# Kernel optimization log

Hardware: AMD Instinct MI355X
Metric: run time of the kernel (lower is better)

The kernel has to match this reference:

```python
import jax, jax.numpy as jnp
import numpy as np

NEG_INF = -9e15  # same masking constant as the torch module


def setup_inputs() -> dict:
    key = jax.random.key(0)
    k1, k2, k3 = jax.random.split(key, 3)
    B, S, F = 8, 2048, 128
    H, D = 4, 32  # n_heads, head_dim = out_features // n_heads
    features = jax.random.normal(k1, (B, S, F), dtype=jnp.float32)
    adj_matrix = jax.random.randint(k2, (B, S, S), 0, 2, dtype=jnp.int32)
    # Xavier-uniform-ish init for W [H, F, D]
    limit = float(np.sqrt(6.0 / (F + D)))
    W = jax.random.uniform(k3, (H, F, D), dtype=jnp.float32, minval=-limit, maxval=limit)
    return {"features": features, "adj_matrix": adj_matrix, "W": W}


def reference(features, adj_matrix, W):
    # features: [B, S, F], adj_matrix: [B, S, S] (>0 == edge), W: [H, F, D]
    D = W.shape[-1]
    Wh = jnp.einsum("bsf,hfd->bhsd", features, W)                 # [B, H, S, D]
    scores = jnp.einsum("bhsd,bhtd->bhst", Wh, Wh) / jnp.sqrt(jnp.float32(D))
    scores = jnp.where(adj_matrix[:, None, :, :] > 0, scores, NEG_INF)
    attn = jax.nn.softmax(scores, axis=-1)                         # [B, H, S, S]
    # dropout is identity at inference (training=False)
    h = jnp.einsum("bhst,bhtd->bhsd", attn, Wh)                    # [B, H, S, D]
    B, H, S, _ = h.shape
    # concat heads along feature dim, matching torch.cat(heads, dim=2)
    return jnp.transpose(h, (0, 2, 1, 3)).reshape(B, S, H * D)
```

## Files before the change

kernel.cpp:

```cpp
#include <hip/hip_runtime.h>
#include <hip/hip_bf16.h>
#include <stdint.h>


namespace {
constexpr int S = 2048;
constexpr int F = 128;
constexpr int H = 4;
constexpr int D = 32;

typedef __attribute__((ext_vector_type(4))) float f32x4;
typedef __attribute__((ext_vector_type(8))) short s16x8;
typedef __attribute__((ext_vector_type(4))) short s16x4;

__device__ __forceinline__ short f2bf(float f) {
  __hip_bfloat16 h = __float2bfloat16(f);
  short s; __builtin_memcpy(&s, &h, sizeof(s)); return s;
}
__device__ __forceinline__ float bf2f(short s) {
  __hip_bfloat16 h; __builtin_memcpy(&h, &s, sizeof(s));
  return __bfloat162float(h);
}

__global__ __launch_bounds__(256) void gat_proj(const float* __restrict__ feat,
                                                const float* __restrict__ W,
                                                short* __restrict__ Wh,
                                                short* __restrict__ WhT) {
  __shared__ __align__(16) short ftile[64][136];
  const int tid = threadIdx.x;
  const int w = tid >> 6;
  const int l = tid & 63;
  const int ln = l & 15, lg = l >> 4, g4 = (l >> 4) * 4;
  const int row0 = blockIdx.x * 64;
  const int b = row0 >> 11;
  const int sl0 = row0 & (S - 1);

#pragma unroll
  for (int i = 0; i < 4; ++i) {
    int c = i * 256 + tid;
    int r = c >> 4, c8 = (c & 15) * 8;
    const float* src = feat + (size_t)(row0 + r) * F + c8;
    float4 v0 = *(const float4*)src;
    float4 v1 = *(const float4*)(src + 4);
    s16x8 v;
    v[0]=f2bf(v0.x); v[1]=f2bf(v0.y); v[2]=f2bf(v0.z); v[3]=f2bf(v0.w);
    v[4]=f2bf(v1.x); v[5]=f2bf(v1.y); v[6]=f2bf(v1.z); v[7]=f2bf(v1.w);
    *(s16x8*)&ftile[r][c8] = v;
  }

  s16x8 bfr[4][2];
#pragma unroll
  for (int ks = 0; ks < 4; ++ks)
#pragma unroll
    for (int nt = 0; nt < 2; ++nt) {
      s16x8 v;
#pragma unroll
      for (int j = 0; j < 8; ++j)
        v[j] = f2bf(W[((size_t)w * F + ks*32 + lg*8 + j) * D + nt*16 + ln]);
      bfr[ks][nt] = v;
    }
  __syncthreads();

  const f32x4 z4 = {0.f, 0.f, 0.f, 0.f};
#pragma unroll
  for (int mt = 0; mt < 4; ++mt) {
    s16x8 a[4];
#pragma unroll
    for (int ks = 0; ks < 4; ++ks)
      a[ks] = *(const s16x8*)&ftile[mt*16 + ln][ks*32 + lg*8];
#pragma unroll
    for (int nt = 0; nt < 2; ++nt) {
      f32x4 c = z4;
#pragma unroll
      for (int ks = 0; ks < 4; ++ks)
        c = __builtin_amdgcn_mfma_f32_16x16x32_bf16(a[ks], bfr[ks][nt], c, 0, 0, 0);
      s16x4 tv;
#pragma unroll
      for (int r = 0; r < 4; ++r) {
        tv[r] = f2bf(c[r]);
        int srow = row0 + mt*16 + g4 + r;
        int s = srow & (S - 1);
        Wh[(((size_t)b * H + w) * S + s) * D + nt*16 + ln] = tv[r];
      }
      *(s16x4*)&WhT[(((size_t)b * H + w) * D + nt*16 + ln) * S + sl0 + mt*16 + g4] = tv;
    }
  }
}

__global__ __launch_bounds__(256, 2) void gat_attn(const int* __restrict__ adj,
                                                   const short* __restrict__ Wh,
                                                   const short* __restrict__ WhT,
                                                   float* __restrict__ out) {
  __shared__ unsigned adjw[2][32][20];
  __shared__ __align__(16) short ptl[H][32][64];

  const int tid = threadIdx.x;
  const int w = tid >> 6;
  const int l = tid & 63;
  const int ln = l & 15, lg = l >> 4, g4 = (l >> 4) * 4;
  const int e3 = ln & 7;
  const int b = blockIdx.x >> 6;
  const int s0 = (blockIdx.x & 63) * 32;

  const short* WhBH = Wh + ((size_t)b * H + w) * S * D;
  const short* WhTBH = WhT + ((size_t)b * H + w) * D * S;
  const int* adjB = adj + (size_t)b * S * S;
  short* pw = &ptl[w][0][0];

  const int ra = tid >> 4;
  const int cg = tid & 15;
  const int* adjR0 = adjB + (size_t)(s0 + ra) * S + cg * 4;
  const int* adjR1 = adjB + (size_t)(s0 + 16 + ra) * S + cg * 4;

  const float cs = 0.25503486f;
  s16x8 qf[2];
#pragma unroll
  for (int qt = 0; qt < 2; ++qt) {
    s16x8 v = *(const s16x8*)&WhBH[(size_t)(s0 + qt*16 + ln) * D + lg*8];
    s16x8 o;
#pragma unroll
    for (int j = 0; j < 8; ++j) o[j] = f2bf(bf2f(v[j]) * cs);
    qf[qt] = o;
  }

  const f32x4 z4 = {0.f, 0.f, 0.f, 0.f};
  f32x4 accO[2][2];
#pragma unroll
  for (int i = 0; i < 2; ++i)
#pragma unroll
    for (int j = 0; j < 2; ++j) accO[i][j] = z4;
  float psum[2] = {0.f, 0.f};

  int4 a0 = *(const int4*)adjR0;
  int4 a1 = *(const int4*)adjR1;
  s16x8 kf[4];
#pragma unroll
  for (int mt = 0; mt < 4; ++mt)
    kf[mt] = *(const s16x8*)&WhBH[(size_t)(mt*16 + ln) * D + lg*8];
  s16x8 av[2][2];
#pragma unroll
  for (int dt = 0; dt < 2; ++dt)
#pragma unroll
    for (int kt = 0; kt < 2; ++kt)
      av[dt][kt] = *(const s16x8*)&WhTBH[(size_t)(dt*16 + ln) * S + kt*32 + lg*8];
  adjw[0][ra][cg]      = (unsigned)a0.x | ((unsigned)a0.y << 8) |
                         ((unsigned)a0.z << 16) | ((unsigned)a0.w << 24);
  adjw[0][16 + ra][cg] = (unsigned)a1.x | ((unsigned)a1.y << 8) |
                         ((unsigned)a1.z << 16) | ((unsigned)a1.w << 24);
  __syncthreads();

#pragma unroll 1
  for (int it = 0; it < S / 64; ++it) {
    const int cur = it & 1, nxt = cur ^ 1;
    const int t0n = (it + 1) * 64;
    const bool pf = (it < S / 64 - 1);

    int4 a0n, a1n;
    s16x8 kn[4], avn[2][2];
    if (pf) {
      a0n = *(const int4*)(adjR0 + t0n);
      a1n = *(const int4*)(adjR1 + t0n);
#pragma unroll
      for (int mt = 0; mt < 4; ++mt)
        kn[mt] = *(const s16x8*)&WhBH[(size_t)(t0n + mt*16 + ln) * D + lg*8];
#pragma unroll
      for (int dt = 0; dt < 2; ++dt)
#pragma unroll
        for (int kt = 0; kt < 2; ++kt)
          avn[dt][kt] = *(const s16x8*)&WhTBH[(size_t)(dt*16 + ln) * S + t0n + kt*32 + lg*8];
    }

    f32x4 accS[4][2];
#pragma unroll
    for (int mt = 0; mt < 4; ++mt)
#pragma unroll
      for (int qt = 0; qt < 2; ++qt)
        accS[mt][qt] = __builtin_amdgcn_mfma_f32_16x16x32_bf16(kf[mt], qf[qt], z4, 0, 0, 0);

#pragma unroll
    for (int qt = 0; qt < 2; ++qt) {
      const unsigned* ab = &adjw[cur][qt*16 + ln][lg];
#pragma unroll
      for (int mt = 0; mt < 4; ++mt) {
        unsigned m = ab[mt*4];
        f32x4 sv = accS[mt][qt];
        float p0 = (m & 0xffu)       ? __builtin_amdgcn_exp2f(sv[0]) : 0.f;
        float p1 = (m & 0xff00u)     ? __builtin_amdgcn_exp2f(sv[1]) : 0.f;
        float p2 = (m & 0xff0000u)   ? __builtin_amdgcn_exp2f(sv[2]) : 0.f;
        float p3 = (m & 0xff000000u) ? __builtin_amdgcn_exp2f(sv[3]) : 0.f;
        psum[qt] += (p0 + p1) + (p2 + p3);
        s16x4 pk;
        pk[0] = f2bf(p0); pk[1] = f2bf(p1); pk[2] = f2bf(p2); pk[3] = f2bf(p3);
        int pg = mt*2 + (lg >> 1);
        *(s16x4*)&pw[(qt*16 + ln)*64 + ((pg ^ e3) << 3) + (lg & 1)*4] = pk;
      }
    }

    s16x8 ap[2][2];
#pragma unroll
    for (int qt = 0; qt < 2; ++qt)
#pragma unroll
      for (int kt = 0; kt < 2; ++kt)
        ap[qt][kt] = *(const s16x8*)&pw[(qt*16 + ln)*64 + (((kt*4 + lg) ^ e3) << 3)];

#pragma unroll
    for (int dt = 0; dt < 2; ++dt)
#pragma unroll
      for (int qt = 0; qt < 2; ++qt)
#pragma unroll
        for (int kt = 0; kt < 2; ++kt)
          accO[dt][qt] = __builtin_amdgcn_mfma_f32_16x16x32_bf16(
              av[dt][kt], ap[qt][kt], accO[dt][qt], 0, 0, 0);

    if (pf) {
      adjw[nxt][ra][cg]      = (unsigned)a0n.x | ((unsigned)a0n.y << 8) |
                               ((unsigned)a0n.z << 16) | ((unsigned)a0n.w << 24);
      adjw[nxt][16 + ra][cg] = (unsigned)a1n.x | ((unsigned)a1n.y << 8) |
                               ((unsigned)a1n.z << 16) | ((unsigned)a1n.w << 24);
#pragma unroll
      for (int mt = 0; mt < 4; ++mt) kf[mt] = kn[mt];
#pragma unroll
      for (int dt = 0; dt < 2; ++dt)
#pragma unroll
        for (int kt = 0; kt < 2; ++kt) av[dt][kt] = avn[dt][kt];
    }
    __syncthreads();
  }

#pragma unroll
  for (int qt = 0; qt < 2; ++qt) {
    psum[qt] += __shfl_xor(psum[qt], 16, 64);
    psum[qt] += __shfl_xor(psum[qt], 32, 64);
  }
#pragma unroll
  for (int qt = 0; qt < 2; ++qt) {
    float inv = 1.0f / psum[qt];
#pragma unroll
    for (int dt = 0; dt < 2; ++dt) {
      f32x4 o;
#pragma unroll
      for (int r = 0; r < 4; ++r) o[r] = accO[dt][qt][r] * inv;
      *(f32x4*)&out[((size_t)b * S + s0 + qt*16 + ln) * (H * D) + w*32 + dt*16 + g4] = o;
    }
  }
}

}

extern "C" void kernel_launch(void* const* d_in, const int* in_sizes, int n_in,
                              void* d_out, int out_size, void* d_ws, size_t ws_size,
                              hipStream_t stream) {
  const float* feat = (const float*)d_in[0];
  const int* adj    = (const int*)d_in[1];
  const float* W    = (const float*)d_in[2];
  float* out        = (float*)d_out;
  short* Wh         = (short*)d_ws;
  short* WhT        = (short*)d_ws + (size_t)8 * H * S * D;

  gat_proj<<<(8 * S) / 64, 256, 0, stream>>>(feat, W, Wh, WhT);
  gat_attn<<<8 * (S / 32), 256, 0, stream>>>(adj, Wh, WhT, out);
}
```

Baseline: 68.94 us.

## Split attention key dimension across blocks with partial-sum reduce kernel

Splits the key loop of the attention kernel into up to 4 chunks handled by separate blocks, writing unnormalized partial outputs and row sums to workspace, then combines them in a new reduce kernel. This raises the block count from 512 to up to 2048 to fill more of the GPU's compute units, and the launch bound now targets 4 blocks per CU. Block IDs are remapped, and the adjacency mask is now stored in shared memory as float 0/1 values, so masking becomes a multiply instead of a branch. The cost is extra workspace traffic, a third kernel launch, and a larger shared-memory mask tile.

```diff
diff --git a/kernel.cpp b/kernel.cpp
--- a/kernel.cpp
+++ b/kernel.cpp
@@ -20,6 +20,12 @@
 __device__ __forceinline__ float bf2f(short s) {
   __hip_bfloat16 h; __builtin_memcpy(&h, &s, sizeof(s));
   return __bfloat162float(h);
+}
+__device__ __forceinline__ f32x4 i4mask(int4 a) {
+  f32x4 r;
+  r[0] = a.x ? 1.0f : 0.0f; r[1] = a.y ? 1.0f : 0.0f;
+  r[2] = a.z ? 1.0f : 0.0f; r[3] = a.w ? 1.0f : 0.0f;
+  return r;
 }
 
 __global__ __launch_bounds__(256) void gat_proj(const float* __restrict__ feat,
@@ -87,11 +93,14 @@
   }
 }
 
-__global__ __launch_bounds__(256, 2) void gat_attn(const int* __restrict__ adj,
+__global__ __launch_bounds__(256, 4) void gat_attn(const int* __restrict__ adj,
                                                    const short* __restrict__ Wh,
                                                    const short* __restrict__ WhT,
-                                                   float* __restrict__ out) {
-  __shared__ unsigned adjw[2][32][20];
+                                                   float* __restrict__ out,
+                                                   float* __restrict__ PO,
+                                                   float* __restrict__ PS,
+                                                   int tiles) {
+  __shared__ __align__(16) float adjf[2][32][68];
   __shared__ __align__(16) short ptl[H][32][64];
 
   const int tid = threadIdx.x;
@@ -99,18 +108,25 @@
   const int l = tid & 63;
   const int ln = l & 15, lg = l >> 4, g4 = (l >> 4) * 4;
   const int e3 = ln & 7;
-  const int b = blockIdx.x >> 6;
-  const int s0 = (blockIdx.x & 63) * 32;
+
+  const int N = gridDim.x;
+  const int rbid = ((int)blockIdx.x & 7) * (N >> 3) + ((int)blockIdx.x >> 3);
+  const int c = rbid >> 9;
+  const int g = rbid & 511;
+  const int b = g >> 6;
+  const int s0 = (g & 63) * 32;
+  const int it0 = c * tiles;
 
   const short* WhBH = Wh + ((size_t)b * H + w) * S * D;
   const short* WhTBH = WhT + ((size_t)b * H + w) * D * S;
-  const int* adjB = adj + (size_t)b * S * S;
+  const int* adjBase = adj + (size_t)b * S * S;
   short* pw = &ptl[w][0][0];
 
-  const int ra = tid >> 4;
-  const int cg = tid & 15;
-  const int* adjR0 = adjB + (size_t)(s0 + ra) * S + cg * 4;
-  const int* adjR1 = adjB + (size_t)(s0 + 16 + ra) * S + cg * 4;
+  const int arow = tid >> 3;
+  const int ga = ((tid & 7) + arow) & 7;
+  const int gb = ga + 8;
+  const int* adjA = adjBase + (size_t)(s0 + arow) * S + it0*64 + ga*4;
+  const int* adjBp = adjBase + (size_t)(s0 + arow) * S + it0*64 + gb*4;
 
   const float cs = 0.25503486f;
   s16x8 qf[2];
@@ -131,38 +147,41 @@
     for (int j = 0; j < 2; ++j) accO[i][j] = z4;
   float psum[2] = {0.f, 0.f};
 
-  int4 a0 = *(const int4*)adjR0;
-  int4 a1 = *(const int4*)adjR1;
+  {
+    int4 a0 = *(const int4*)adjA;
+    int4 a1 = *(const int4*)adjBp;
+    *(f32x4*)&adjf[0][arow][ga*4] = i4mask(a0);
+    *(f32x4*)&adjf[0][arow][gb*4] = i4mask(a1);
+  }
   s16x8 kf[4];
-#pragma unroll
-  for (int mt = 0; mt < 4; ++mt)
-    kf[mt] = *(const s16x8*)&WhBH[(size_t)(mt*16 + ln) * D + lg*8];
   s16x8 av[2][2];
-#pragma unroll
-  for (int dt = 0; dt < 2; ++dt)
-#pragma unroll
-    for (int kt = 0; kt < 2; ++kt)
-      av[dt][kt] = *(const s16x8*)&WhTBH[(size_t)(dt*16 + ln) * S + kt*32 + lg*8];
-  adjw[0][ra][cg]      = (unsigned)a0.x | ((unsigned)a0.y << 8) |
-                         ((unsigned)a0.z << 16) | ((unsigned)a0.w << 24);
-  adjw[0][16 + ra][cg] = (unsigned)a1.x | ((unsigned)a1.y << 8) |
-                         ((unsigned)a1.z << 16) | ((unsigned)a1.w << 24);
+  {
+    const size_t t0 = (size_t)it0 * 64;
+#pragma unroll
+    for (int mt = 0; mt < 4; ++mt)
+      kf[mt] = *(const s16x8*)&WhBH[(t0 + mt*16 + ln) * D + lg*8];
+#pragma unroll
+    for (int dt = 0; dt < 2; ++dt)
+#pragma unroll
+      for (int kt = 0; kt < 2; ++kt)
+        av[dt][kt] = *(const s16x8*)&WhTBH[(size_t)(dt*16 + ln) * S + t0 + kt*32 + lg*8];
+  }
   __syncthreads();
 
 #pragma unroll 1
-  for (int it = 0; it < S / 64; ++it) {
-    const int cur = it & 1, nxt = cur ^ 1;
-    const int t0n = (it + 1) * 64;
-    const bool pf = (it < S / 64 - 1);
+  for (int i = 0; i < tiles; ++i) {
+    const int cur = i & 1, nxt = cur ^ 1;
+    const bool pf = (i < tiles - 1);
+    const size_t t0n = (size_t)(it0 + i + 1) * 64;
 
     int4 a0n, a1n;
     s16x8 kn[4], avn[2][2];
     if (pf) {
-      a0n = *(const int4*)(adjR0 + t0n);
-      a1n = *(const int4*)(adjR1 + t0n);
+      a0n = *(const int4*)(adjA + (i + 1) * 64);
+      a1n = *(const int4*)(adjBp + (i + 1) * 64);
 #pragma unroll
       for (int mt = 0; mt < 4; ++mt)
-        kn[mt] = *(const s16x8*)&WhBH[(size_t)(t0n + mt*16 + ln) * D + lg*8];
+        kn[mt] = *(const s16x8*)&WhBH[(t0n + mt*16 + ln) * D + lg*8];
 #pragma unroll
       for (int dt = 0; dt < 2; ++dt)
 #pragma unroll
@@ -179,15 +198,15 @@
 
 #pragma unroll
     for (int qt = 0; qt < 2; ++qt) {
-      const unsigned* ab = &adjw[cur][qt*16 + ln][lg];
+      const float* ar = &adjf[cur][qt*16 + ln][0];
 #pragma unroll
       for (int mt = 0; mt < 4; ++mt) {
-        unsigned m = ab[mt*4];
+        f32x4 mv = *(const f32x4*)&ar[(mt*4 + lg)*4];
         f32x4 sv = accS[mt][qt];
-        float p0 = (m & 0xffu)       ? __builtin_amdgcn_exp2f(sv[0]) : 0.f;
-        float p1 = (m & 0xff00u)     ? __builtin_amdgcn_exp2f(sv[1]) : 0.f;
-        float p2 = (m & 0xff0000u)   ? __builtin_amdgcn_exp2f(sv[2]) : 0.f;
-        float p3 = (m & 0xff000000u) ? __builtin_amdgcn_exp2f(sv[3]) : 0.f;
+        float p0 = __builtin_amdgcn_exp2f(sv[0]) * mv[0];
+        float p1 = __builtin_amdgcn_exp2f(sv[1]) * mv[1];
+        float p2 = __builtin_amdgcn_exp2f(sv[2]) * mv[2];
+        float p3 = __builtin_amdgcn_exp2f(sv[3]) * mv[3];
         psum[qt] += (p0 + p1) + (p2 + p3);
         s16x4 pk;
         pk[0] = f2bf(p0); pk[1] = f2bf(p1); pk[2] = f2bf(p2); pk[3] = f2bf(p3);
@@ -213,10 +232,8 @@
               av[dt][kt], ap[qt][kt], accO[dt][qt], 0, 0, 0);
 
     if (pf) {
-      adjw[nxt][ra][cg]      = (unsigned)a0n.x | ((unsigned)a0n.y << 8) |
-                               ((unsigned)a0n.z << 16) | ((unsigned)a0n.w << 24);
-      adjw[nxt][16 + ra][cg] = (unsigned)a1n.x | ((unsigned)a1n.y << 8) |
-                               ((unsigned)a1n.z << 16) | ((unsigned)a1n.w << 24);
+      *(f32x4*)&adjf[nxt][arow][ga*4] = i4mask(a0n);
+      *(f32x4*)&adjf[nxt][arow][gb*4] = i4mask(a1n);
 #pragma unroll
       for (int mt = 0; mt < 4; ++mt) kf[mt] = kn[mt];
 #pragma unroll
@@ -232,17 +249,54 @@
     psum[qt] += __shfl_xor(psum[qt], 16, 64);
     psum[qt] += __shfl_xor(psum[qt], 32, 64);
   }
-#pragma unroll
-  for (int qt = 0; qt < 2; ++qt) {
-    float inv = 1.0f / psum[qt];
-#pragma unroll
-    for (int dt = 0; dt < 2; ++dt) {
-      f32x4 o;
-#pragma unroll
-      for (int r = 0; r < 4; ++r) o[r] = accO[dt][qt][r] * inv;
-      *(f32x4*)&out[((size_t)b * S + s0 + qt*16 + ln) * (H * D) + w*32 + dt*16 + g4] = o;
-    }
-  }
+
+  if (PO == nullptr) {
+#pragma unroll
+    for (int qt = 0; qt < 2; ++qt) {
+      float inv = 1.0f / psum[qt];
+#pragma unroll
+      for (int dt = 0; dt < 2; ++dt) {
+        f32x4 o;
+#pragma unroll
+        for (int r = 0; r < 4; ++r) o[r] = accO[dt][qt][r] * inv;
+        *(f32x4*)&out[((size_t)b * S + s0 + qt*16 + ln) * (H * D) + w*32 + dt*16 + g4] = o;
+      }
+    }
+  } else {
+    const size_t pbase = (size_t)rbid * H + w;
+    float* po = PO + pbase * 1024;
+#pragma unroll
+    for (int qt = 0; qt < 2; ++qt) {
+#pragma unroll
+      for (int dt = 0; dt < 2; ++dt)
+        *(f32x4*)&po[(qt*16 + ln)*32 + dt*16 + g4] = accO[dt][qt];
+      if (lg == 0) PS[pbase * 32 + qt*16 + ln] = psum[qt];
+    }
+  }
+}
+
+__global__ __launch_bounds__(256) void gat_reduce(const float* __restrict__ PO,
+                                                  const float* __restrict__ PS,
+                                                  float* __restrict__ out,
+                                                  int nchunks) {
+  const int f4 = blockIdx.x * 256 + threadIdx.x;
+  const int d4 = f4 & 31;
+  const int h = d4 >> 3;
+  const int dq = d4 & 7;
+  const int s_flat = f4 >> 5;
+  const int b = s_flat >> 11, s = s_flat & 2047;
+  const int g = b * 64 + (s >> 5), q = s & 31;
+
+  f32x4 acc = {0.f, 0.f, 0.f, 0.f};
+  float ps = 0.f;
+  for (int c = 0; c < nchunks; ++c) {
+    size_t pbase = ((size_t)(c * 512 + g)) * H + h;
+    acc += *(const f32x4*)&PO[pbase * 1024 + q*32 + dq*4];
+    ps += PS[pbase * 32 + q];
+  }
+  float inv = 1.0f / ps;
+  f32x4 o = acc * inv;
+  *(f32x4*)&out[(size_t)f4 * 4] = o;
 }
 
 }
@@ -254,9 +308,25 @@
   const int* adj    = (const int*)d_in[1];
   const float* W    = (const float*)d_in[2];
   float* out        = (float*)d_out;
-  short* Wh         = (short*)d_ws;
-  short* WhT        = (short*)d_ws + (size_t)8 * H * S * D;
+
+  short* Wh  = (short*)d_ws;
+  short* WhT = Wh + (size_t)8 * H * S * D;
+  const size_t whbytes = (size_t)2 * 8 * H * S * D * sizeof(short);
+  const size_t chunkPO = (size_t)512 * H * 1024 * sizeof(float);
+  const size_t chunkPS = (size_t)512 * H * 32 * sizeof(float);
+
+  int nchunks = 1;
+  if (ws_size >= whbytes + 4 * (chunkPO + chunkPS)) nchunks = 4;
+  else if (ws_size >= whbytes + 2 * (chunkPO + chunkPS)) nchunks = 2;
+
+  float* PO = nullptr;
+  float* PS = nullptr;
+  if (nchunks > 1) {
+    PO = (float*)((char*)d_ws + whbytes);
+    PS = (float*)((char*)d_ws + whbytes + (size_t)nchunks * chunkPO);
+  }
 
   gat_proj<<<(8 * S) / 64, 256, 0, stream>>>(feat, W, Wh, WhT);
-  gat_attn<<<8 * (S / 32), 256, 0, stream>>>(adj, Wh, WhT, out);
-}
+  gat_attn<<<512 * nchunks, 256, 0, stream>>>(adj, Wh, WhT, out, PO, PS, 32 / nchunks);
+  if (nchunks > 1) gat_reduce<<<2048, 256, 0, stream>>>(PO, PS, out, nchunks);
+}
```

Result: slower. 268.9 us (+290.1%).
